# Performance work log

Hardware: AMD Instinct MI355X
Metric: run time of the kernel (lower is better)

The kernel has to match this reference:

```python
import jax, jax.numpy as jnp
import numpy as np

M = 64; N_SC = 32; SPS = 8; LENCP = 16; NUMOFDM = 256 // N_SC
BETA = 0.5; SPAN = 16; LENRRC = SPAN * SPS + 1  # 129
FC = 25e6; FS = 10e6 * SPS
CLIP = 1.2; SNR = 10.0; THRES = 8.0
LEN_T = NUMOFDM * (M + LENCP)              # 640
NUMSAMPLES = LEN_T * SPS + LENRRC * 2      # 5378
L1 = LEN_T * SPS + LENRRC - 1              # 5248 (post pulse-shaping length)


def make_rrc():
    # standard root-raised-cosine, unit energy
    t = np.arange(-SPAN * SPS // 2, SPAN * SPS // 2 + 1) / SPS
    h = np.zeros_like(t)
    eps = 1e-9
    t0 = np.abs(t) < eps
    ts = np.abs(np.abs(t) - 1.0 / (4 * BETA)) < eps
    reg = ~(t0 | ts)
    tr = t[reg]
    h[reg] = (np.sin(np.pi * tr * (1 - BETA)) + 4 * BETA * tr * np.cos(np.pi * tr * (1 + BETA))) / (
        np.pi * tr * (1 - (4 * BETA * tr) ** 2))
    h[t0] = 1 + BETA * (4 / np.pi - 1)
    h[ts] = (BETA / np.sqrt(2)) * ((1 + 2 / np.pi) * np.sin(np.pi / (4 * BETA)) +
                                   (1 - 2 / np.pi) * np.cos(np.pi / (4 * BETA)))
    h = h / np.sqrt(np.sum(h ** 2))
    return h.astype(np.float32)


def _conv_full(u, k):
    # torch F.conv1d(x, k.flip(), padding=K-1) == full convolution with k
    K = k.shape[0]
    return jax.lax.conv_general_dilated(
        u[:, None, :], k[::-1][None, None, :], (1,), [(K - 1, K - 1)],
        dimension_numbers=('NCH', 'OIH', 'NCH'))[:, 0, :]


def _pulse_filter(c, rrc):
    return _conv_full(c.real, rrc) + 1j * _conv_full(c.imag, rrc)


def _power_norm(z):
    m = jnp.mean(z, axis=1, keepdims=True)
    s = jnp.std(z, axis=1, ddof=1, keepdims=True)  # torch.std is unbiased
    return (z - m) / (s + 1e-8)


def _forward(x, W_enc, b_enc, W_dec, b_dec, rrc, awgn, startloc):
    B = x.shape[0]
    # --- encoder (linear proxy for ResNetTx) -> 512 reals ---
    z = x.reshape(B, -1) @ W_enc + b_enc
    z = _power_norm(z)
    c = z.reshape(B, 256, 2)
    c = (c[..., 0] + 1j * c[..., 1]).reshape(B, NUMOFDM, N_SC)  # complex64
    # --- DFT precoding ---
    c = jnp.fft.fftshift(jnp.fft.fft(c, axis=-1, norm='ortho'), axes=-1)
    # --- subcarrier mapping (contiguous block, mapping==1) ---
    loc = jnp.arange(startloc, startloc + N_SC)
    data_f = jnp.zeros((B, NUMOFDM, M), jnp.complex64).at[:, :, loc].set(c)
    data_t = jnp.fft.ifft(data_f, axis=-1, norm='ortho')
    data_t = jnp.concatenate([data_t[:, :, -LENCP:], data_t], axis=-1)  # CP
    data_t = data_t.reshape(B, LEN_T)
    # --- zero-stuffed upsampling + RRC pulse shaping ---
    over = jnp.zeros((B, LEN_T * SPS), jnp.complex64).at[:, ::SPS].set(data_t)
    xc = _pulse_filter(over, rrc)  # (B, L1)
    # --- carrier mixing ---
    n = jnp.arange(NUMSAMPLES, dtype=jnp.float32)
    cos_c = jnp.sqrt(2.0) * jnp.cos(2 * jnp.pi * FC * n / FS)
    sin_c = jnp.sqrt(2.0) * jnp.sin(2 * jnp.pi * FC * n / FS)
    data_x = xc.real * cos_c[:L1] - xc.imag * sin_c[:L1]
    # --- clipping ---
    thr = CLIP * jnp.sqrt(jnp.mean(jnp.square(data_x), axis=1, keepdims=True))
    over_amp = jax.nn.relu(jnp.abs(data_x) - thr)
    data_x = (1.0 - over_amp / (jnp.abs(data_x) + 1e-8)) * data_x
    # --- PAPR ---
    tstart = (LENRRC + 1) // 2
    p = jnp.square(data_x[:, tstart:tstart + LEN_T * SPS])
    PAPRdB = 10.0 * jnp.log10(jnp.max(p, axis=1) / jnp.mean(p, axis=1))
    PAPRloss = jnp.mean(jax.nn.relu(PAPRdB - THRES))
    # --- AWGN channel (no fading) ---
    data_r = data_x + awgn
    # --- downconversion + matched filter ---
    rc = data_r * cos_c[:L1] - 1j * (data_r * sin_c[:L1])
    filt = _pulse_filter(rc, rrc)  # (B, L1 + LENRRC - 1) = (B, 5376)
    y = filt[:, LENRRC - 1:filt.shape[1] - LENRRC:SPS]  # (B, LEN_T)
    y = y.reshape(B, NUMOFDM, M + LENCP)[:, :, LENCP:]
    y = jnp.fft.fft(y, axis=-1, norm='ortho')[:, :, loc]
    y = jnp.fft.ifft(jnp.fft.fftshift(y, axes=-1), axis=-1, norm='ortho')
    y = y.reshape(B, NUMOFDM * N_SC)
    y = jnp.stack([y.real, y.imag], axis=-1).reshape(B, 8, 8, 8)
    # --- decoder (linear proxy for ResNetRx) ---
    out = (y.reshape(B, 512) @ W_dec + b_dec).reshape(B, 3, 32, 32)
    return out, PAPRdB, PAPRloss


def setup_inputs() -> dict:
    key = jax.random.key(0)
    ks = jax.random.split(key, 4)
    B = 1024
    x = jax.random.normal(ks[0], (B, 3, 32, 32), jnp.float32)
    W_enc = jax.random.normal(ks[1], (3072, 512), jnp.float32) * 0.02
    b_enc = jnp.zeros((512,), jnp.float32)
    W_dec = jax.random.normal(ks[2], (512, 3072), jnp.float32) * 0.05
    b_dec = jnp.zeros((3072,), jnp.float32)
    rrc = jnp.asarray(make_rrc())
    noise_std = 10.0 ** (-SNR / 20.0)
    awgn = jax.random.normal(ks[3], (B, L1), jnp.float32) * noise_std
    return {"x": x, "W_enc": W_enc, "b_enc": b_enc, "W_dec": W_dec,
            "b_dec": b_dec, "rrc": rrc, "awgn": awgn, "startloc": 7}


def reference(x, W_enc, b_enc, W_dec, b_dec, rrc, awgn, startloc):
    return _forward(x, W_enc, b_enc, W_dec, b_dec, rrc, awgn, startloc)
```

## Files before the change

kernel.cpp:

```cpp
#include <hip/hip_runtime.h>
#include <hip/hip_bf16.h>
#include <math.h>

#define L1_     5248
#define LENRRC_ 129
#define TSTART_ 65
#define NWIN_   5120
#define SWZ(m) ((m) + ((m) >> 3))

typedef __attribute__((ext_vector_type(8))) short s16x8;
typedef __attribute__((ext_vector_type(4))) float f32x4;

__device__ inline ushort bf16_rne(float x) {
    unsigned xb = __float_as_uint(x);
    return (ushort)((xb + 0x7fffu + ((xb >> 16) & 1u)) >> 16);
}

__device__ inline float wave_sum(float v) {
    #pragma unroll
    for (int m = 32; m > 0; m >>= 1) v += __shfl_xor(v, m, 64);
    return v;
}
__device__ inline float wave_max(float v) {
    #pragma unroll
    for (int m = 32; m > 0; m >>= 1) v = fmaxf(v, __shfl_xor(v, m, 64));
    return v;
}

__device__ inline void gl_lds16(const void* g, void* l) {
    __builtin_amdgcn_global_load_lds(
        (const __attribute__((address_space(1))) unsigned int*)g,
        (__attribute__((address_space(3))) unsigned int*)l, 16, 0, 0);
}

__global__ __launch_bounds__(256) void pack_k(const float* __restrict__ x,
        const float* __restrict__ W1, const float* __restrict__ W2,
        const float* __restrict__ benc,
        ushort* __restrict__ xb, ushort* __restrict__ w1t, ushort* __restrict__ w2t,
        float* __restrict__ z)
{
    __shared__ ushort tile[64][70];
    const int blk = blockIdx.x, tid = threadIdx.x;
    if (blk < 3072) {
        int i = blk * 256 + tid;
        float4 v = ((const float4*)x)[i];
        ushort4 h;
        h.x = bf16_rne(v.x); h.y = bf16_rne(v.y);
        h.z = bf16_rne(v.z); h.w = bf16_rne(v.w);
        ((ushort4*)xb)[i] = h;
    } else if (blk < 3840) {
        const float* W; ushort* T; int K, N, n0, k0;
        if (blk < 3456) {
            int idx = blk - 3072;
            W = W1; T = w1t; K = 3072; N = 512;
            n0 = (idx & 7) * 64; k0 = (idx >> 3) * 64;
        } else {
            int idx = blk - 3456;
            W = W2; T = w2t; K = 512; N = 3072;
            n0 = (idx % 48) * 64; k0 = (idx / 48) * 64;
        }
        const int cr = tid >> 4, cc = (tid & 15) * 4;
        #pragma unroll
        for (int i = 0; i < 4; ++i) {
            int kk = i * 16 + cr;
            float4 v = *(const float4*)&W[(size_t)(k0 + kk) * N + n0 + cc];
            tile[kk][cc]     = bf16_rne(v.x);
            tile[kk][cc + 1] = bf16_rne(v.y);
            tile[kk][cc + 2] = bf16_rne(v.z);
            tile[kk][cc + 3] = bf16_rne(v.w);
        }
        __syncthreads();
        #pragma unroll
        for (int i = 0; i < 4; ++i) {
            int nn = i * 16 + cr;
            ushort4 h;
            h.x = tile[cc][nn]; h.y = tile[cc + 1][nn];
            h.z = tile[cc + 2][nn]; h.w = tile[cc + 3][nn];
            *(ushort4*)&T[(size_t)(n0 + nn) * K + k0 + cc] = h;
        }
    } else {
        int i = (blk - 3840) * 256 + tid;
        z[i] = benc[i & 511];
    }
}

__global__ __launch_bounds__(256) void gemm1_k(const ushort* __restrict__ Ab,
        const ushort* __restrict__ Bb, float* __restrict__ C, int M, int N, int K,
        int partial)
{
    __shared__ __attribute__((aligned(16))) ushort Asl[64 * 64];
    __shared__ __attribute__((aligned(16))) ushort Bsl[128 * 64];
    const int tid = threadIdx.x;
    const int lane = tid & 63, wave = tid >> 6;
    const int wm = (wave >> 1) * 32, wn = (wave & 1) * 64;
    const int m0 = blockIdx.y * 64, n0 = blockIdx.x * 128;
    const int kch = K / 8, kbeg = blockIdx.z * kch, kend = kbeg + kch;
    const int fm = lane & 15, q = lane >> 4;
    f32x4 acc[2][4] = {};

    int arow[2], akb[2], brow[4], bkb[4];
    #pragma unroll
    for (int j = 0; j < 2; ++j) {
        int c = ((wave * 2 + j) << 6) + lane;
        arow[j] = c >> 3; akb[j] = (c & 7) ^ (arow[j] & 7);
    }
    #pragma unroll
    for (int j = 0; j < 4; ++j) {
        int c = ((wave * 4 + j) << 6) + lane;
        brow[j] = c >> 3; bkb[j] = (c & 7) ^ (brow[j] & 7);
    }

    for (int kt = kbeg; kt < kend; kt += 64) {
        #pragma unroll
        for (int j = 0; j < 2; ++j)
            gl_lds16(&Ab[(size_t)(m0 + arow[j]) * K + kt + akb[j] * 8],
                     &Asl[(wave * 2 + j) << 9]);
        #pragma unroll
        for (int j = 0; j < 4; ++j)
            gl_lds16(&Bb[(size_t)(n0 + brow[j]) * K + kt + bkb[j] * 8],
                     &Bsl[(wave * 4 + j) << 9]);
        __syncthreads();
        #pragma unroll
        for (int ks = 0; ks < 2; ++ks) {
            s16x8 a[2], b[4];
            #pragma unroll
            for (int mf = 0; mf < 2; ++mf) {
                int r = wm + mf * 16 + fm;
                a[mf] = *(const s16x8*)&Asl[(r << 6) + ((((ks << 2) + q) ^ (r & 7)) << 3)];
            }
            #pragma unroll
            for (int nf = 0; nf < 4; ++nf) {
                int r = wn + nf * 16 + fm;
                b[nf] = *(const s16x8*)&Bsl[(r << 6) + ((((ks << 2) + q) ^ (r & 7)) << 3)];
            }
            #pragma unroll
            for (int mf = 0; mf < 2; ++mf)
                #pragma unroll
                for (int nf = 0; nf < 4; ++nf)
                    acc[mf][nf] = __builtin_amdgcn_mfma_f32_16x16x32_bf16(a[mf], b[nf], acc[mf][nf], 0, 0, 0);
        }
        __syncthreads();
    }

    if (partial) {
        float* Cs = C + (size_t)blockIdx.z * ((size_t)M * N);
        #pragma unroll
        for (int mf = 0; mf < 2; ++mf)
            #pragma unroll
            for (int nf = 0; nf < 4; ++nf)
                #pragma unroll
                for (int r = 0; r < 4; ++r) {
                    int m = m0 + wm + mf * 16 + q * 4 + r;
                    int n = n0 + wn + nf * 16 + fm;
                    Cs[(size_t)m * N + n] = acc[mf][nf][r];
                }
    } else {
        #pragma unroll
        for (int mf = 0; mf < 2; ++mf)
            #pragma unroll
            for (int nf = 0; nf < 4; ++nf)
                #pragma unroll
                for (int r = 0; r < 4; ++r) {
                    int m = m0 + wm + mf * 16 + q * 4 + r;
                    int n = n0 + wn + nf * 16 + fm;
                    atomicAdd(&C[(size_t)m * N + n], acc[mf][nf][r]);
                }
    }
}

__global__ __launch_bounds__(256) void gemm2_k(const ushort* __restrict__ Ab,
        const ushort* __restrict__ Bb, const float* __restrict__ bias,
        const float* __restrict__ papr, float* __restrict__ C,
        float* __restrict__ out_loss, int M, int N, int K)
{
    __shared__ __attribute__((aligned(16))) ushort Asl[64 * 64];
    __shared__ __attribute__((aligned(16))) ushort Bsl[64 * 64];
    __shared__ float red[4];
    const int tid = threadIdx.x;
    const int lane = tid & 63, wave = tid >> 6;
    const int wm = (wave >> 1) * 32, wn = (wave & 1) * 32;
    const int m0 = blockIdx.y * 64, n0 = blockIdx.x * 64;
    const int fm = lane & 15, q = lane >> 4;
    f32x4 acc[2][2] = {};

    int srow[2], skb[2];
    #pragma unroll
    for (int j = 0; j < 2; ++j) {
        int c = ((wave * 2 + j) << 6) + lane;
        srow[j] = c >> 3; skb[j] = (c & 7) ^ (srow[j] & 7);
    }

    for (int kt = 0; kt < K; kt += 64) {
        #pragma unroll
        for (int j = 0; j < 2; ++j) {
            gl_lds16(&Ab[(size_t)(m0 + srow[j]) * K + kt + skb[j] * 8],
                     &Asl[(wave * 2 + j) << 9]);
            gl_lds16(&Bb[(size_t)(n0 + srow[j]) * K + kt + skb[j] * 8],
                     &Bsl[(wave * 2 + j) << 9]);
        }
        __syncthreads();
        #pragma unroll
        for (int ks = 0; ks < 2; ++ks) {
            s16x8 a[2], b[2];
            #pragma unroll
            for (int mf = 0; mf < 2; ++mf) {
                int r = wm + mf * 16 + fm;
                a[mf] = *(const s16x8*)&Asl[(r << 6) + ((((ks << 2) + q) ^ (r & 7)) << 3)];
            }
            #pragma unroll
            for (int nf = 0; nf < 2; ++nf) {
                int r = wn + nf * 16 + fm;
                b[nf] = *(const s16x8*)&Bsl[(r << 6) + ((((ks << 2) + q) ^ (r & 7)) << 3)];
            }
            #pragma unroll
            for (int mf = 0; mf < 2; ++mf)
                #pragma unroll
                for (int nf = 0; nf < 2; ++nf)
                    acc[mf][nf] = __builtin_amdgcn_mfma_f32_16x16x32_bf16(a[mf], b[nf], acc[mf][nf], 0, 0, 0);
        }
        __syncthreads();
    }

    #pragma unroll
    for (int mf = 0; mf < 2; ++mf)
        #pragma unroll
        for (int nf = 0; nf < 2; ++nf)
            #pragma unroll
            for (int r = 0; r < 4; ++r) {
                int m = m0 + wm + mf * 16 + q * 4 + r;
                int n = n0 + wn + nf * 16 + fm;
                C[(size_t)m * N + n] = acc[mf][nf][r] + bias[n];
            }

    if (blockIdx.x == 0 && blockIdx.y == 0) {
        float s = 0.f;
        for (int i = tid; i < 1024; i += 256) { float v = papr[i] - 8.f; s += v > 0.f ? v : 0.f; }
        s = wave_sum(s);
        if (lane == 0) red[wave] = s;
        __syncthreads();
        if (tid == 0) *out_loss = (red[0] + red[1] + red[2] + red[3]) * (1.f / 1024.f);
    }
}

__global__ __launch_bounds__(512, 4) void mega_k(const float* __restrict__ z,
        const float* __restrict__ benc,
        const float* __restrict__ rrc, const float* __restrict__ awgn,
        const int* __restrict__ slocp, ushort* __restrict__ y5b,
        float* __restrict__ papr, float* __restrict__ out_papr, int nsp)
{
    __shared__ float  zl[2][512];
    __shared__ float2 frfi[2][8][32];
    __shared__ float2 trti[2][672];
    __shared__ float  hl[132];
    __shared__ float  csl[16], ssl[16];
    __shared__ float2 cs64[64];
    __shared__ __attribute__((aligned(16))) float2 gcs[130];
    __shared__ float  dxr[2][SWZ(L1_ - 1) + 1];
    __shared__ float  red[2][8], red2[2][8];

    const int b0 = blockIdx.x * 2, b1 = b0 + 1;
    const int tid = threadIdx.x;
    const int lane = tid & 63, wv = tid >> 6;
    const int sloc = *slocp;

    if (tid < 64) {
        float ang = 0.09817477042468103f * (float)tid;
        float s, c; sincosf(ang, &s, &c);
        cs64[tid] = make_float2(c, s);
    }
    if (tid >= 64 && tid < 80) {
        int t = tid - 64;
        float ang = 1.9634954084936207f * (float)t;
        float s, c; sincosf(ang, &s, &c);
        csl[t] = 1.4142135623730951f * c; ssl[t] = 1.4142135623730951f * s;
    }
    if (tid >= 96 && tid < 160) {
        int t = (tid - 96) & 31, row = (tid - 96) >> 5;
        int idx = (t < 16) ? t : (640 + t);
        trti[row][idx] = make_float2(0.f, 0.f);
    }
    if (tid >= 256 && tid < 256 + LENRRC_) hl[tid - 256] = rrc[tid - 256];

    float va, vb;
    if (nsp) {
        va = benc[tid]; vb = va;
        const float* zp0 = z + (size_t)b0 * 512;
        const float* zp1 = z + (size_t)b1 * 512;
        for (int s = 0; s < nsp; ++s) {
            va += zp0[(size_t)s * 524288 + tid];
            vb += zp1[(size_t)s * 524288 + tid];
        }
    } else {
        va = z[(size_t)b0 * 512 + tid];
        vb = z[(size_t)b1 * 512 + tid];
    }
    __syncthreads();

    if (tid < LENRRC_) {
        int neg = (16 - (tid & 15)) & 15;
        gcs[tid] = make_float2(hl[tid] * csl[neg], hl[tid] * ssl[neg]);
    }

    {
        float S0 = wave_sum(va), Q0 = wave_sum(va * va);
        float S1 = wave_sum(vb), Q1 = wave_sum(vb * vb);
        if (lane == 0) { red[0][wv] = S0; red2[0][wv] = Q0; red[1][wv] = S1; red2[1][wv] = Q1; }
    }
    __syncthreads();
    {
        float S0 = 0.f, Q0 = 0.f, S1 = 0.f, Q1 = 0.f;
        #pragma unroll
        for (int w = 0; w < 8; ++w) {
            S0 += red[0][w]; Q0 += red2[0][w];
            S1 += red[1][w]; Q1 += red2[1][w];
        }
        float m0 = S0 * (1.f / 512.f), m1 = S1 * (1.f / 512.f);
        float i0 = 1.f / (sqrtf((Q0 - S0 * m0) * (1.f / 511.f)) + 1e-8f);
        float i1 = 1.f / (sqrtf((Q1 - S1 * m1) * (1.f / 511.f)) + 1e-8f);
        zl[0][tid] = (va - m0) * i0;
        zl[1][tid] = (vb - m1) * i1;
    }
    __syncthreads();

    if (tid < 256) {
        int s = tid >> 5, kk = tid & 31;
        int kk2 = (kk + 16) & 31;
        float sr0 = 0.f, si0 = 0.f, sr1 = 0.f, si1 = 0.f;
        int t2 = 0;
        #pragma unroll 4
        for (int q = 0; q < 32; ++q) {
            float2 w = cs64[2 * t2];
            float2 c0 = *(const float2*)&zl[0][(s * 32 + q) * 2];
            float2 c1 = *(const float2*)&zl[1][(s * 32 + q) * 2];
            sr0 += c0.x * w.x + c0.y * w.y;
            si0 += c0.y * w.x - c0.x * w.y;
            sr1 += c1.x * w.x + c1.y * w.y;
            si1 += c1.y * w.x - c1.x * w.y;
            t2 = (t2 + kk2) & 31;
        }
        const float sc = 0.1767766952966369f;
        frfi[0][s][kk] = make_float2(sr0 * sc, si0 * sc);
        frfi[1][s][kk] = make_float2(sr1 * sc, si1 * sc);
    }
    __syncthreads();

    if (tid < 256) {
        int s = tid >> 5, n = tid & 31;
        float er0 = 0.f, ei0 = 0.f, o_r0 = 0.f, o_i0 = 0.f;
        float er1 = 0.f, ei1 = 0.f, o_r1 = 0.f, o_i1 = 0.f;
        int t = (sloc * n) & 63;
        #pragma unroll 2
        for (int k = 0; k < 32; k += 2) {
            float2 w = cs64[t];
            float2 f0 = frfi[0][s][k], f1 = frfi[1][s][k];
            er0 += f0.x * w.x - f0.y * w.y;
            ei0 += f0.y * w.x + f0.x * w.y;
            er1 += f1.x * w.x - f1.y * w.y;
            ei1 += f1.y * w.x + f1.x * w.y;
            t = (t + n) & 63;
            w = cs64[t];
            f0 = frfi[0][s][k + 1]; f1 = frfi[1][s][k + 1];
            o_r0 += f0.x * w.x - f0.y * w.y;
            o_i0 += f0.y * w.x + f0.x * w.y;
            o_r1 += f1.x * w.x - f1.y * w.y;
            o_i1 += f1.y * w.x + f1.x * w.y;
            t = (t + n) & 63;
        }
        float sgn = (sloc & 1) ? -1.f : 1.f;
        int base = s * 80;
        {
            float dr0 = (er0 + o_r0) * 0.125f, di0 = (ei0 + o_i0) * 0.125f;
            float dr1 = sgn * (er0 - o_r0) * 0.125f, di1 = sgn * (ei0 - o_i0) * 0.125f;
            trti[0][base + 32 + n] = make_float2(dr0, di0);
            trti[0][base + 64 + n] = make_float2(dr1, di1);
            if (n >= 16) trti[0][base + n] = make_float2(dr1, di1);
        }
        {
            float dr0 = (er1 + o_r1) * 0.125f, di0 = (ei1 + o_i1) * 0.125f;
            float dr1 = sgn * (er1 - o_r1) * 0.125f, di1 = sgn * (ei1 - o_i1) * 0.125f;
            trti[1][base + 32 + n] = make_float2(dr0, di0);
            trti[1][base + 64 + n] = make_float2(dr1, di1);
            if (n >= 16) trti[1][base + n] = make_float2(dr1, di1);
        }
    }
    __syncthreads();

    float ss0 = 0.f, ss1 = 0.f;
    for (int tsk = tid; tsk < 1312; tsk += 512) {
        int a = tsk >> 1, g = tsk & 1;
        float ar0[4] = {}, ai0[4] = {}, ar1[4] = {}, ai1[4] = {};
        #pragma unroll 4
        for (int d = 0; d < 16; ++d) {
            float2 t0 = trti[0][16 + a - d];
            float2 t1 = trti[1][16 + a - d];
            #pragma unroll
            for (int r = 0; r < 4; ++r) {
                float h = hl[g * 4 + r + 8 * d];
                ar0[r] += t0.x * h; ai0[r] += t0.y * h;
                ar1[r] += t1.x * h; ai1[r] += t1.y * h;
            }
        }
        if (g == 0) {
            float2 t0 = trti[0][a], t1 = trti[1][a];
            float h = hl[128];
            ar0[0] += t0.x * h; ai0[0] += t0.y * h;
            ar1[0] += t1.x * h; ai1[0] += t1.y * h;
        }
        int cb = (a & 1) * 8;
        #pragma unroll
        for (int r = 0; r < 4; ++r) {
            int rr = g * 4 + r;
            float cv = csl[cb + rr], sv = ssl[cb + rr];
            float v0 = ar0[r] * cv - ai0[r] * sv;
            float v1 = ar1[r] * cv - ai1[r] * sv;
            dxr[0][SWZ(a * 8 + rr)] = v0;
            dxr[1][SWZ(a * 8 + rr)] = v1;
            ss0 += v0 * v0; ss1 += v1 * v1;
        }
    }
    ss0 = wave_sum(ss0); ss1 = wave_sum(ss1);
    if (lane == 0) { red[0][wv] = ss0; red[1][wv] = ss1; }
    __syncthreads();
    float thr0, thr1;
    {
        float S0 = 0.f, S1 = 0.f;
        #pragma unroll
        for (int w = 0; w < 8; ++w) { S0 += red[0][w]; S1 += red[1][w]; }
        thr0 = 1.2f * sqrtf(S0 / (float)L1_);
        thr1 = 1.2f * sqrtf(S1 / (float)L1_);
    }
    __syncthreads();

    float pm0 = 0.f, ps0 = 0.f, pm1 = 0.f, ps1 = 0.f;
    {
        const float4* ag0 = (const float4*)&awgn[(size_t)b0 * L1_];
        const float4* ag1 = (const float4*)&awgn[(size_t)b1 * L1_];
        for (int ii = tid; ii < 1312; ii += 512) {
            float4 a0 = ag0[ii], a1 = ag1[ii];
            int i = ii * 4;
            #pragma unroll
            for (int e = 0; e < 4; ++e) {
                int idx = i + e;
                bool win = (idx >= TSTART_ && idx < TSTART_ + NWIN_);
                float aw0 = (e == 0) ? a0.x : (e == 1) ? a0.y : (e == 2) ? a0.z : a0.w;
                float aw1 = (e == 0) ? a1.x : (e == 1) ? a1.y : (e == 2) ? a1.z : a1.w;
                {
                    float x = dxr[0][SWZ(idx)];
                    float ax = fabsf(x);
                    float over = fmaxf(ax - thr0, 0.f);
                    float y = (1.f - over / (ax + 1e-8f)) * x;
                    if (win) { float p = y * y; ps0 += p; pm0 = fmaxf(pm0, p); }
                    dxr[0][SWZ(idx)] = y + aw0;
                }
                {
                    float x = dxr[1][SWZ(idx)];
                    float ax = fabsf(x);
                    float over = fmaxf(ax - thr1, 0.f);
                    float y = (1.f - over / (ax + 1e-8f)) * x;
                    if (win) { float p = y * y; ps1 += p; pm1 = fmaxf(pm1, p); }
                    dxr[1][SWZ(idx)] = y + aw1;
                }
            }
        }
    }
    ps0 = wave_sum(ps0); pm0 = wave_max(pm0);
    ps1 = wave_sum(ps1); pm1 = wave_max(pm1);
    if (lane == 0) { red[0][wv] = ps0; red2[0][wv] = pm0; red[1][wv] = ps1; red2[1][wv] = pm1; }
    __syncthreads();
    if (tid == 0) {
        float s0 = 0.f, m0 = 0.f, s1 = 0.f, m1 = 0.f;
        #pragma unroll
        for (int w = 0; w < 8; ++w) {
            s0 += red[0][w]; m0 = fmaxf(m0, red2[0][w]);
            s1 += red[1][w]; m1 = fmaxf(m1, red2[1][w]);
        }
        float p0 = 10.f * log10f(m0 / (s0 / (float)NWIN_));
        float p1 = 10.f * log10f(m1 / (s1 / (float)NWIN_));
        papr[b0] = p0; out_papr[b0] = p0;
        papr[b1] = p1; out_papr[b1] = p1;
    }
    __syncthreads();

    {
        int s = wv, n = lane;
        int T0 = s * 80 + n + 32;
        int base = 9 * T0;
        float ar0 = 0.f, ai0 = 0.f, ar1 = 0.f, ai1 = 0.f;
        int db = 0;
        #pragma unroll 4
        for (int e = 0; e < 16; ++e) {
            float4 g01 = *(const float4*)&gcs[db];
            float4 g23 = *(const float4*)&gcs[db + 2];
            float4 g45 = *(const float4*)&gcs[db + 4];
            float4 g67 = *(const float4*)&gcs[db + 6];
            float gx[8] = { g01.x, g01.z, g23.x, g23.z, g45.x, g45.z, g67.x, g67.z };
            float gy[8] = { g01.y, g01.w, g23.y, g23.w, g45.y, g45.w, g67.y, g67.w };
            #pragma unroll
            for (int u = 0; u < 8; ++u) {
                int off = (u == 0) ? 0 : (u + 1);
                float v0 = dxr[0][base - off];
                float v1 = dxr[1][base - off];
                ar0 += v0 * gx[u]; ai0 += v0 * gy[u];
                ar1 += v1 * gx[u]; ai1 += v1 * gy[u];
            }
            base -= 9; db += 8;
        }
        {
            float2 g = gcs[128];
            float v0 = dxr[0][base], v1 = dxr[1][base];
            ar0 += v0 * g.x; ai0 += v0 * g.y;
            ar1 += v1 * g.x; ai1 += v1 * g.y;
        }
        bool odd = (n & 1);
        float dx0 = odd ? -ar0 : ar0, dy0 = odd ? ai0 : -ai0;
        float dx1 = odd ? -ar1 : ar1, dy1 = odd ? ai1 : -ai1;
        float px0 = __shfl_xor(dx0, 32, 64), py0 = __shfl_xor(dy0, 32, 64);
        float px1 = __shfl_xor(dx1, 32, 64), py1 = __shfl_xor(dy1, 32, 64);
        float2 r0 = (n < 32) ? make_float2(dx0 + px0, dy0 + py0)
                             : make_float2(px0 - dx0, py0 - dy0);
        float2 r1 = (n < 32) ? make_float2(dx1 + px1, dy1 + py1)
                             : make_float2(px1 - dx1, py1 - dy1);
        int di = ((n >> 5) * 256) + s * 32 + (n & 31);
        trti[0][di] = r0;
        trti[1][di] = r1;
    }
    __syncthreads();

    if (tid < 256) {
        int s = tid >> 5, kk = tid & 31;
        int f = sloc + kk;
        int doff = ((f & 1) ? 256 : 0) + s * 32;
        const float2* d0 = &trti[0][doff];
        const float2* d1 = &trti[1][doff];
        float vr0 = 0.f, vi0 = 0.f, vr1 = 0.f, vi1 = 0.f;
        int t = 0;
        #pragma unroll 4
        for (int n = 0; n < 32; ++n) {
            float2 w = cs64[t];
            float2 e0 = d0[n], e1 = d1[n];
            vr0 += e0.x * w.x + e0.y * w.y;
            vi0 += e0.y * w.x - e0.x * w.y;
            vr1 += e1.x * w.x + e1.y * w.y;
            vi1 += e1.y * w.x - e1.x * w.y;
            t = (t + f) & 63;
        }
        int ksh = (kk + 16) & 31;
        frfi[0][s][ksh] = make_float2(vr0 * 0.125f, vi0 * 0.125f);
        frfi[1][s][ksh] = make_float2(vr1 * 0.125f, vi1 * 0.125f);
    }
    __syncthreads();

    if (tid < 256) {
        int s = tid >> 5, q2 = tid & 31;
        float ur0 = 0.f, ui0 = 0.f, ur1 = 0.f, ui1 = 0.f;
        int t2 = 0;
        #pragma unroll 4
        for (int k = 0; k < 32; ++k) {
            float2 w = cs64[2 * t2];
            float2 f0 = frfi[0][s][k], f1 = frfi[1][s][k];
            ur0 += f0.x * w.x - f0.y * w.y;
            ui0 += f0.y * w.x + f0.x * w.y;
            ur1 += f1.x * w.x - f1.y * w.y;
            ui1 += f1.y * w.x + f1.x * w.y;
            t2 = (t2 + q2) & 31;
        }
        const float sc = 0.1767766952966369f;
        ushort2 h0; h0.x = bf16_rne(ur0 * sc); h0.y = bf16_rne(ui0 * sc);
        ushort2 h1; h1.x = bf16_rne(ur1 * sc); h1.y = bf16_rne(ui1 * sc);
        *(ushort2*)&y5b[(size_t)b0 * 512 + (s * 32 + q2) * 2] = h0;
        *(ushort2*)&y5b[(size_t)b1 * 512 + (s * 32 + q2) * 2] = h1;
    }
}

extern "C" void kernel_launch(void* const* d_in, const int* in_sizes, int n_in,
                              void* d_out, int out_size, void* d_ws, size_t ws_size,
                              hipStream_t stream) {
    const float* x    = (const float*)d_in[0];
    const float* Wenc = (const float*)d_in[1];
    const float* benc = (const float*)d_in[2];
    const float* Wdec = (const float*)d_in[3];
    const float* bdec = (const float*)d_in[4];
    const float* rrc  = (const float*)d_in[5];
    const float* awgn = (const float*)d_in[6];
    const int* sloc   = (const int*)d_in[7];
    float* out = (float*)d_out;

    char* wsb = (char*)d_ws;
    ushort* xb   = (ushort*)wsb;                     wsb += (size_t)1024 * 3072 * 2;
    ushort* w1t  = (ushort*)wsb;                     wsb += (size_t)512 * 3072 * 2;
    ushort* w2t  = (ushort*)wsb;                     wsb += (size_t)3072 * 512 * 2;
    ushort* y5b  = (ushort*)wsb;                     wsb += (size_t)1024 * 512 * 2;
    float*  papr = (float*)wsb;                      wsb += 1024 * 4;
    float*  zbuf = (float*)wsb;
    size_t head = (size_t)((char*)zbuf - (char*)d_ws);
    int partial = (ws_size >= head + (size_t)8 * 1024 * 512 * 4) ? 1 : 0;

    float* out_papr = out + (size_t)1024 * 3072;
    float* out_loss = out_papr + 1024;

    pack_k<<<partial ? 3840 : 5888, 256, 0, stream>>>(x, Wenc, Wdec, benc, xb, w1t, w2t, zbuf);
    gemm1_k<<<dim3(4, 16, 8), 256, 0, stream>>>(xb, w1t, zbuf, 1024, 512, 3072, partial);
    mega_k<<<512, 512, 0, stream>>>(zbuf, benc, rrc, awgn, sloc, y5b, papr, out_papr,
                                    partial ? 8 : 0);
    gemm2_k<<<dim3(48, 16, 1), 256, 0, stream>>>(y5b, w2t, bdec, papr, out, out_loss, 1024, 3072, 512);
}
```

Before: 147.7 us.

## Fuse x bf16 conversion into gemm1 and replace DFT chains with cotangent-kernel transforms

The input x is no longer packed to bf16 in a separate pass. gemm1 now loads fp32 x directly, rounds it to bf16 and stores it into LDS, which removes a full read/write round trip of the activation matrix. In mega_k, the encoder-side and receiver-side DFT/IDFT pairs are collapsed into a single closed-form step per stage, using a precomputed cotangent table. This drops the frfi intermediate stages and their barriers, and all 512 threads now participate instead of 256. In exchange, gemm1 issues plain vector loads for A instead of asynchronous global-to-LDS loads, and the new algebraic formulation may change numerical rounding.

```diff
diff --git a/kernel.cpp b/kernel.cpp
--- a/kernel.cpp
+++ b/kernel.cpp
@@ -33,29 +33,20 @@
         (__attribute__((address_space(3))) unsigned int*)l, 16, 0, 0);
 }
 
-__global__ __launch_bounds__(256) void pack_k(const float* __restrict__ x,
-        const float* __restrict__ W1, const float* __restrict__ W2,
-        const float* __restrict__ benc,
-        ushort* __restrict__ xb, ushort* __restrict__ w1t, ushort* __restrict__ w2t,
-        float* __restrict__ z)
+__global__ __launch_bounds__(256) void pack_k(const float* __restrict__ W1,
+        const float* __restrict__ W2, const float* __restrict__ benc,
+        ushort* __restrict__ w1t, ushort* __restrict__ w2t, float* __restrict__ z)
 {
     __shared__ ushort tile[64][70];
     const int blk = blockIdx.x, tid = threadIdx.x;
-    if (blk < 3072) {
-        int i = blk * 256 + tid;
-        float4 v = ((const float4*)x)[i];
-        ushort4 h;
-        h.x = bf16_rne(v.x); h.y = bf16_rne(v.y);
-        h.z = bf16_rne(v.z); h.w = bf16_rne(v.w);
-        ((ushort4*)xb)[i] = h;
-    } else if (blk < 3840) {
+    if (blk < 768) {
         const float* W; ushort* T; int K, N, n0, k0;
-        if (blk < 3456) {
-            int idx = blk - 3072;
+        if (blk < 384) {
+            int idx = blk;
             W = W1; T = w1t; K = 3072; N = 512;
             n0 = (idx & 7) * 64; k0 = (idx >> 3) * 64;
         } else {
-            int idx = blk - 3456;
+            int idx = blk - 384;
             W = W2; T = w2t; K = 512; N = 3072;
             n0 = (idx % 48) * 64; k0 = (idx / 48) * 64;
         }
@@ -79,12 +70,12 @@
             *(ushort4*)&T[(size_t)(n0 + nn) * K + k0 + cc] = h;
         }
     } else {
-        int i = (blk - 3840) * 256 + tid;
+        int i = (blk - 768) * 256 + tid;
         z[i] = benc[i & 511];
     }
 }
 
-__global__ __launch_bounds__(256) void gemm1_k(const ushort* __restrict__ Ab,
+__global__ __launch_bounds__(256) void gemm1_k(const float* __restrict__ Ax,
         const ushort* __restrict__ Bb, float* __restrict__ C, int M, int N, int K,
         int partial)
 {
@@ -112,13 +103,22 @@
 
     for (int kt = kbeg; kt < kend; kt += 64) {
         #pragma unroll
-        for (int j = 0; j < 2; ++j)
-            gl_lds16(&Ab[(size_t)(m0 + arow[j]) * K + kt + akb[j] * 8],
-                     &Asl[(wave * 2 + j) << 9]);
-        #pragma unroll
         for (int j = 0; j < 4; ++j)
             gl_lds16(&Bb[(size_t)(n0 + brow[j]) * K + kt + bkb[j] * 8],
                      &Bsl[(wave * 4 + j) << 9]);
+        #pragma unroll
+        for (int j = 0; j < 2; ++j) {
+            int c = ((wave * 2 + j) << 6) + lane;
+            const float* src = &Ax[(size_t)(m0 + arow[j]) * K + kt + akb[j] * 8];
+            float4 v0 = *(const float4*)src;
+            float4 v1 = *(const float4*)(src + 4);
+            s16x8 hv;
+            hv[0] = (short)bf16_rne(v0.x); hv[1] = (short)bf16_rne(v0.y);
+            hv[2] = (short)bf16_rne(v0.z); hv[3] = (short)bf16_rne(v0.w);
+            hv[4] = (short)bf16_rne(v1.x); hv[5] = (short)bf16_rne(v1.y);
+            hv[6] = (short)bf16_rne(v1.z); hv[7] = (short)bf16_rne(v1.w);
+            *(s16x8*)&Asl[c * 8] = hv;
+        }
         __syncthreads();
         #pragma unroll
         for (int ks = 0; ks < 2; ++ks) {
@@ -249,11 +249,11 @@
         float* __restrict__ papr, float* __restrict__ out_papr, int nsp)
 {
     __shared__ float  zl[2][512];
-    __shared__ float2 frfi[2][8][32];
     __shared__ float2 trti[2][672];
     __shared__ float  hl[132];
     __shared__ float  csl[16], ssl[16];
     __shared__ float2 cs64[64];
+    __shared__ float  ct[64];
     __shared__ __attribute__((aligned(16))) float2 gcs[130];
     __shared__ float  dxr[2][SWZ(L1_ - 1) + 1];
     __shared__ float  red[2][8], red2[2][8];
@@ -262,6 +262,7 @@
     const int tid = threadIdx.x;
     const int lane = tid & 63, wv = tid >> 6;
     const int sloc = *slocp;
+    const float S2048 = 0.02209708691207961f;
 
     if (tid < 64) {
         float ang = 0.09817477042468103f * (float)tid;
@@ -278,6 +279,12 @@
         int t = (tid - 96) & 31, row = (tid - 96) >> 5;
         int idx = (t < 16) ? t : (640 + t);
         trti[row][idx] = make_float2(0.f, 0.f);
+    }
+    if (tid >= 160 && tid < 224) {
+        int j = tid - 160;
+        float v = 0.f;
+        if (j & 1) { float s, c; sincosf(0.04908738521234052f * (float)j, &s, &c); v = c / s; }
+        ct[j] = v;
     }
     if (tid >= 256 && tid < 256 + LENRRC_) hl[tid - 256] = rrc[tid - 256];
 
@@ -317,70 +324,43 @@
         float m0 = S0 * (1.f / 512.f), m1 = S1 * (1.f / 512.f);
         float i0 = 1.f / (sqrtf((Q0 - S0 * m0) * (1.f / 511.f)) + 1e-8f);
         float i1 = 1.f / (sqrtf((Q1 - S1 * m1) * (1.f / 511.f)) + 1e-8f);
-        zl[0][tid] = (va - m0) * i0;
-        zl[1][tid] = (vb - m1) * i1;
-    }
-    __syncthreads();
-
-    if (tid < 256) {
-        int s = tid >> 5, kk = tid & 31;
-        int kk2 = (kk + 16) & 31;
-        float sr0 = 0.f, si0 = 0.f, sr1 = 0.f, si1 = 0.f;
-        int t2 = 0;
+        float sg = ((tid >> 1) & 1) ? -1.f : 1.f;
+        zl[0][tid] = (va - m0) * i0 * sg;
+        zl[1][tid] = (vb - m1) * i1 * sg;
+    }
+    __syncthreads();
+
+    {
+        int r = tid >> 8, t = tid & 255;
+        int s = t >> 5, j = t & 31;
+        int base = s * 80;
+        const float2* zs = (const float2*)&zl[r][s * 64];
+        int n = 2 * j + 1;
+        float Zr = 0.f, Zi = 0.f, Tr = 0.f, Ti = 0.f;
         #pragma unroll 4
         for (int q = 0; q < 32; ++q) {
-            float2 w = cs64[2 * t2];
-            float2 c0 = *(const float2*)&zl[0][(s * 32 + q) * 2];
-            float2 c1 = *(const float2*)&zl[1][(s * 32 + q) * 2];
-            sr0 += c0.x * w.x + c0.y * w.y;
-            si0 += c0.y * w.x - c0.x * w.y;
-            sr1 += c1.x * w.x + c1.y * w.y;
-            si1 += c1.y * w.x - c1.x * w.y;
-            t2 = (t2 + kk2) & 31;
-        }
-        const float sc = 0.1767766952966369f;
-        frfi[0][s][kk] = make_float2(sr0 * sc, si0 * sc);
-        frfi[1][s][kk] = make_float2(sr1 * sc, si1 * sc);
-    }
-    __syncthreads();
-
-    if (tid < 256) {
-        int s = tid >> 5, n = tid & 31;
-        float er0 = 0.f, ei0 = 0.f, o_r0 = 0.f, o_i0 = 0.f;
-        float er1 = 0.f, ei1 = 0.f, o_r1 = 0.f, o_i1 = 0.f;
-        int t = (sloc * n) & 63;
-        #pragma unroll 2
-        for (int k = 0; k < 32; k += 2) {
-            float2 w = cs64[t];
-            float2 f0 = frfi[0][s][k], f1 = frfi[1][s][k];
-            er0 += f0.x * w.x - f0.y * w.y;
-            ei0 += f0.y * w.x + f0.x * w.y;
-            er1 += f1.x * w.x - f1.y * w.y;
-            ei1 += f1.y * w.x + f1.x * w.y;
-            t = (t + n) & 63;
-            w = cs64[t];
-            f0 = frfi[0][s][k + 1]; f1 = frfi[1][s][k + 1];
-            o_r0 += f0.x * w.x - f0.y * w.y;
-            o_i0 += f0.y * w.x + f0.x * w.y;
-            o_r1 += f1.x * w.x - f1.y * w.y;
-            o_i1 += f1.y * w.x + f1.x * w.y;
-            t = (t + n) & 63;
-        }
-        float sgn = (sloc & 1) ? -1.f : 1.f;
-        int base = s * 80;
+            float2 a = zs[q];
+            float w = ct[(n - 2 * q) & 63];
+            Zr += a.x; Zi += a.y;
+            Tr += a.x * w; Ti += a.y * w;
+        }
         {
-            float dr0 = (er0 + o_r0) * 0.125f, di0 = (ei0 + o_i0) * 0.125f;
-            float dr1 = sgn * (er0 - o_r0) * 0.125f, di1 = sgn * (ei0 - o_i0) * 0.125f;
-            trti[0][base + 32 + n] = make_float2(dr0, di0);
-            trti[0][base + 64 + n] = make_float2(dr1, di1);
-            if (n >= 16) trti[0][base + n] = make_float2(dr1, di1);
+            float2 cw = cs64[(n * sloc) & 63];
+            float Ar = Zr - Ti, Ai = Zi + Tr;
+            float dr = S2048 * (Ar * cw.x - Ai * cw.y);
+            float di = S2048 * (Ai * cw.x + Ar * cw.y);
+            trti[r][base + 32 + n] = make_float2(dr, di);
+            if (n >= 48) trti[r][base + n - 32] = make_float2(dr, di);
         }
         {
-            float dr0 = (er1 + o_r1) * 0.125f, di0 = (ei1 + o_i1) * 0.125f;
-            float dr1 = sgn * (er1 - o_r1) * 0.125f, di1 = sgn * (ei1 - o_i1) * 0.125f;
-            trti[1][base + 32 + n] = make_float2(dr0, di0);
-            trti[1][base + 64 + n] = make_float2(dr1, di1);
-            if (n >= 16) trti[1][base + n] = make_float2(dr1, di1);
+            int n2 = 2 * j;
+            float2 a = zs[j];
+            float2 cw = cs64[(n2 * sloc) & 63];
+            const float RS2 = 0.7071067811865476f;
+            float dr = RS2 * (a.x * cw.x - a.y * cw.y);
+            float di = RS2 * (a.y * cw.x + a.x * cw.y);
+            trti[r][base + 32 + n2] = make_float2(dr, di);
+            if (n2 >= 48) trti[r][base + n2 - 32] = make_float2(dr, di);
         }
     }
     __syncthreads();
@@ -512,63 +492,32 @@
             ar1 += v1 * g.x; ai1 += v1 * g.y;
         }
         bool odd = (n & 1);
-        float dx0 = odd ? -ar0 : ar0, dy0 = odd ? ai0 : -ai0;
-        float dx1 = odd ? -ar1 : ar1, dy1 = odd ? ai1 : -ai1;
-        float px0 = __shfl_xor(dx0, 32, 64), py0 = __shfl_xor(dy0, 32, 64);
-        float px1 = __shfl_xor(dx1, 32, 64), py1 = __shfl_xor(dy1, 32, 64);
-        float2 r0 = (n < 32) ? make_float2(dx0 + px0, dy0 + py0)
-                             : make_float2(px0 - dx0, py0 - dy0);
-        float2 r1 = (n < 32) ? make_float2(dx1 + px1, dy1 + py1)
-                             : make_float2(px1 - dx1, py1 - dy1);
-        int di = ((n >> 5) * 256) + s * 32 + (n & 31);
-        trti[0][di] = r0;
-        trti[1][di] = r1;
-    }
-    __syncthreads();
-
-    if (tid < 256) {
-        int s = tid >> 5, kk = tid & 31;
-        int f = sloc + kk;
-        int doff = ((f & 1) ? 256 : 0) + s * 32;
-        const float2* d0 = &trti[0][doff];
-        const float2* d1 = &trti[1][doff];
-        float vr0 = 0.f, vi0 = 0.f, vr1 = 0.f, vi1 = 0.f;
-        int t = 0;
+        float wr0 = odd ? -ar0 : ar0, wi0 = odd ? ai0 : -ai0;
+        float wr1 = odd ? -ar1 : ar1, wi1 = odd ? ai1 : -ai1;
+        float2 cw = cs64[(n * sloc) & 63];
+        trti[0][s * 64 + n] = make_float2(wr0 * cw.x + wi0 * cw.y, wi0 * cw.x - wr0 * cw.y);
+        trti[1][s * 64 + n] = make_float2(wr1 * cw.x + wi1 * cw.y, wi1 * cw.x - wr1 * cw.y);
+    }
+    __syncthreads();
+
+    {
+        int r = tid >> 8, t = tid & 255;
+        int s = t >> 5, q = t & 31;
+        const float2* wt = &trti[r][s * 64];
+        float Wr = 0.f, Wi = 0.f, Ur = 0.f, Ui = 0.f;
         #pragma unroll 4
-        for (int n = 0; n < 32; ++n) {
-            float2 w = cs64[t];
-            float2 e0 = d0[n], e1 = d1[n];
-            vr0 += e0.x * w.x + e0.y * w.y;
-            vi0 += e0.y * w.x - e0.x * w.y;
-            vr1 += e1.x * w.x + e1.y * w.y;
-            vi1 += e1.y * w.x - e1.x * w.y;
-            t = (t + f) & 63;
-        }
-        int ksh = (kk + 16) & 31;
-        frfi[0][s][ksh] = make_float2(vr0 * 0.125f, vi0 * 0.125f);
-        frfi[1][s][ksh] = make_float2(vr1 * 0.125f, vi1 * 0.125f);
-    }
-    __syncthreads();
-
-    if (tid < 256) {
-        int s = tid >> 5, q2 = tid & 31;
-        float ur0 = 0.f, ui0 = 0.f, ur1 = 0.f, ui1 = 0.f;
-        int t2 = 0;
-        #pragma unroll 4
-        for (int k = 0; k < 32; ++k) {
-            float2 w = cs64[2 * t2];
-            float2 f0 = frfi[0][s][k], f1 = frfi[1][s][k];
-            ur0 += f0.x * w.x - f0.y * w.y;
-            ui0 += f0.y * w.x + f0.x * w.y;
-            ur1 += f1.x * w.x - f1.y * w.y;
-            ui1 += f1.y * w.x + f1.x * w.y;
-            t2 = (t2 + q2) & 31;
-        }
-        const float sc = 0.1767766952966369f;
-        ushort2 h0; h0.x = bf16_rne(ur0 * sc); h0.y = bf16_rne(ui0 * sc);
-        ushort2 h1; h1.x = bf16_rne(ur1 * sc); h1.y = bf16_rne(ui1 * sc);
-        *(ushort2*)&y5b[(size_t)b0 * 512 + (s * 32 + q2) * 2] = h0;
-        *(ushort2*)&y5b[(size_t)b1 * 512 + (s * 32 + q2) * 2] = h1;
+        for (int u = 0; u < 32; ++u) {
+            float2 a = wt[2 * u + 1];
+            float w = ct[(2 * q - 2 * u - 1) & 63];
+            Wr += a.x; Wi += a.y;
+            Ur += a.x * w; Ui += a.y * w;
+        }
+        float2 e = wt[2 * q];
+        float sgn = (q & 1) ? -S2048 : S2048;
+        float yr = sgn * (32.f * e.x + Wr - Ui);
+        float yi = sgn * (32.f * e.y + Wi + Ur);
+        ushort2 h; h.x = bf16_rne(yr); h.y = bf16_rne(yi);
+        *(ushort2*)&y5b[(size_t)(b0 + r) * 512 + (s * 32 + q) * 2] = h;
     }
 }
 
@@ -586,7 +535,6 @@
     float* out = (float*)d_out;
 
     char* wsb = (char*)d_ws;
-    ushort* xb   = (ushort*)wsb;                     wsb += (size_t)1024 * 3072 * 2;
     ushort* w1t  = (ushort*)wsb;                     wsb += (size_t)512 * 3072 * 2;
     ushort* w2t  = (ushort*)wsb;                     wsb += (size_t)3072 * 512 * 2;
     ushort* y5b  = (ushort*)wsb;                     wsb += (size_t)1024 * 512 * 2;
@@ -598,8 +546,8 @@
     float* out_papr = out + (size_t)1024 * 3072;
     float* out_loss = out_papr + 1024;
 
-    pack_k<<<partial ? 3840 : 5888, 256, 0, stream>>>(x, Wenc, Wdec, benc, xb, w1t, w2t, zbuf);
-    gemm1_k<<<dim3(4, 16, 8), 256, 0, stream>>>(xb, w1t, zbuf, 1024, 512, 3072, partial);
+    pack_k<<<partial ? 768 : 2816, 256, 0, stream>>>(Wenc, Wdec, benc, w1t, w2t, zbuf);
+    gemm1_k<<<dim3(4, 16, 8), 256, 0, stream>>>(x, w1t, zbuf, 1024, 512, 3072, partial);
     mega_k<<<512, 512, 0, stream>>>(zbuf, benc, rrc, awgn, sloc, y5b, papr, out_papr,
                                     partial ? 8 : 0);
     gemm2_k<<<dim3(48, 16, 1), 256, 0, stream>>>(y5b, w2t, bdec, papr, out, out_loss, 1024, 3072, 512);
```

Measured after the change: 145.2 us, median of 2. Within noise of the previous version (-1.7%).
